# Performance work log

Hardware: AMD Instinct MI355X
Metric: run time of the kernel (lower is better)

## Reference

```python
import jax, jax.numpy as jnp
import numpy as np

N_NODES = 50000
N_EDGES = 1600000
BATCH = 1
CHANNELS = 32


def setup_inputs() -> dict:
    key = jax.random.key(0)
    k1, k2, k3, k4 = jax.random.split(key, 4)
    x = jax.random.normal(k1, (BATCH, CHANNELS, N_NODES), dtype=jnp.float32)
    W = jax.random.uniform(k2, (N_NODES,), dtype=jnp.float32)
    iInd = jax.random.randint(k3, (N_EDGES,), 0, N_NODES)
    jInd = jax.random.randint(k4, (N_EDGES,), 0, N_NODES)
    return {"x": x, "W": W, "iInd": iInd, "jInd": jInd, "nnodes": N_NODES}


def reference(x, W, iInd, jInd, nnodes):
    # neighborNode: gather source-node features along edges, weighted by W[iInd]
    # (branch: W.shape[0] == x.shape[2] == nnodes)
    Wi = W[iInd]                      # [E]
    g = Wi * x[:, :, jInd]            # [B, C, E]
    # neighborEdge: scatter-add W[iInd] * g back to target nodes iInd
    # (branch: W.shape[0] == nnodes != E)
    out = jnp.zeros((x.shape[0], x.shape[1], nnodes), dtype=x.dtype)
    out = out.at[:, :, iInd].add(Wi * g)  # [B, C, nnodes]
    return out
```

## Files before the change

kernel.cpp:

```cpp
#include <hip/hip_runtime.h>
#include <math.h>


#define TCH 32
#define BSHIFT 7
#define BNODES 128
#define MAXNB 512
#define SLOTS 32
#define BIN_THREADS 512
#define TILE 4096
#define SR_THREADS 512
#define SPLIT2 4
#define NSUB 32
#define CMP_CAP 1536
#define SJ_CAP 1536

__device__ __forceinline__ unsigned short f32_to_bf16(float f) {
    unsigned int u = __float_as_uint(f);
    unsigned int r = (u + 0x7FFFu + ((u >> 16) & 1u)) >> 16;
    return (unsigned short)r;
}

__global__ void transpose_CN_to_NC_bf16(const float* __restrict__ x,
                                        unsigned short* __restrict__ xtb,
                                        int* __restrict__ gcursor,
                                        int NB, int N) {
    __shared__ float tile[32][33];
    const int tx = threadIdx.x;
    const int ty = threadIdx.y;
    if (blockIdx.x == 0) {
        const int flat = ty * 32 + tx;
        for (int k = flat; k < NB + 1; k += 1024) gcursor[k] = 0;
    }
    const int n0 = blockIdx.x * 32;
    const int n = n0 + tx;
    if (n < N) tile[ty][tx] = x[(size_t)ty * N + n];
    __syncthreads();
    const int nw = n0 + ty;
    if (nw < N) xtb[(size_t)nw * TCH + tx] = f32_to_bf16(tile[tx][ty]);
}

__device__ __forceinline__ void push_ovf(int* ovf_cnt, int2* ovf, int ovf_cap,
                                         int i, int j) {
    const int p = atomicAdd(ovf_cnt, 1);
    if (p < ovf_cap) ovf[p] = make_int2(i, j);
}

__global__ __launch_bounds__(BIN_THREADS) void bin_edges(
    const int* __restrict__ iInd, const int* __restrict__ jInd,
    int* __restrict__ bins, int* __restrict__ gcursor,
    int* __restrict__ ovf_cnt, int2* __restrict__ ovf, int ovf_cap,
    int E, int NB, int cap) {
    __shared__ int stage[MAXNB * SLOTS];
    __shared__ int scnt[MAXNB];
    __shared__ int sums[BIN_THREADS];
    __shared__ unsigned short excl[MAXNB];
    __shared__ unsigned short gbase[MAXNB];
    __shared__ unsigned short bidx[TILE];
    const int tid = threadIdx.x;

    scnt[tid] = 0;
    __syncthreads();

    const int base = blockIdx.x * TILE + tid * 8;
#pragma unroll
    for (int q = 0; q < 2; ++q) {
        const int eb = base + q * 4;
        if (eb + 3 < E) {
            const int4 iv = *(const int4*)(iInd + eb);
            const int4 jv = *(const int4*)(jInd + eb);
            const int is[4] = {iv.x, iv.y, iv.z, iv.w};
            const int js[4] = {jv.x, jv.y, jv.z, jv.w};
#pragma unroll
            for (int k = 0; k < 4; ++k) {
                const int i = is[k], j = js[k];
                const int b = i >> BSHIFT;
                const int slot = atomicAdd(&scnt[b], 1);
                if (slot < SLOTS)
                    stage[b * SLOTS + slot] = ((i & (BNODES - 1)) << 16) | j;
                else
                    push_ovf(ovf_cnt, ovf, ovf_cap, i, j);
            }
        } else {
            for (int k = 0; k < 4; ++k) {
                const int e = eb + k;
                if (e < E) {
                    const int i = iInd[e], j = jInd[e];
                    const int b = i >> BSHIFT;
                    const int slot = atomicAdd(&scnt[b], 1);
                    if (slot < SLOTS)
                        stage[b * SLOTS + slot] = ((i & (BNODES - 1)) << 16) | j;
                    else
                        push_ovf(ovf_cnt, ovf, ovf_cap, i, j);
                }
            }
        }
    }
    __syncthreads();

    const int cb = min(scnt[tid], SLOTS);
    sums[tid] = cb;
    __syncthreads();
    for (int off = 1; off < BIN_THREADS; off <<= 1) {
        const int v = (tid >= off) ? sums[tid - off] : 0;
        __syncthreads();
        sums[tid] += v;
        __syncthreads();
    }
    const int run0 = sums[tid] - cb;
    const int total = sums[BIN_THREADS - 1];
    excl[tid] = (unsigned short)run0;
    if (cb > 0) {
        gbase[tid] = (unsigned short)atomicAdd(&gcursor[tid], cb);
        for (int t = 0; t < cb; ++t)
            bidx[run0 + t] = (unsigned short)tid;
    }
    __syncthreads();

    for (int idx = tid; idx < total; idx += BIN_THREADS) {
        const int b = bidx[idx];
        const int k = idx - (int)excl[b];
        const int rec = stage[b * SLOTS + k];
        const int gslot = (int)gbase[b] + k;
        if (gslot < cap) {
            bins[(size_t)b * cap + gslot] = rec;
        } else {
            push_ovf(ovf_cnt, ovf, ovf_cap,
                     (b << BSHIFT) | (rec >> 16), rec & 0xFFFF);
        }
    }
}

__global__ __launch_bounds__(SR_THREADS) void sort_reduce5(
    const int* __restrict__ bins, const int* __restrict__ gcursor,
    const unsigned short* __restrict__ xtb, const float* __restrict__ W,
    float* __restrict__ out, int* __restrict__ ovf_cnt,
    int2* __restrict__ ovf, int ovf_cap, int N, int cap) {
    const int bucket = blockIdx.x >> 2;
    const int sub = blockIdx.x & (SPLIT2 - 1);
    __shared__ unsigned int cmp[CMP_CAP];
    __shared__ unsigned short sj[SJ_CAP];
    __shared__ float acc[NSUB * 33];
    __shared__ int hcnt[NSUB];
    __shared__ int off2[NSUB + 1];
    __shared__ int cur[NSUB];
    __shared__ int ccnt;

    int cnt = gcursor[bucket];
    if (cnt > cap) cnt = cap;
    const int* rec = bins + (size_t)bucket * cap;

    if (threadIdx.x < NSUB) { hcnt[threadIdx.x] = 0; cur[threadIdx.x] = 0; }
    if (threadIdx.x == 0) ccnt = 0;
    __syncthreads();

    for (int r = threadIdx.x; r < cnt; r += SR_THREADS) {
        const unsigned int pr = (unsigned int)rec[r];
        const int il = (int)(pr >> 16);
        if ((il >> 5) == sub) {
            const int p = atomicAdd(&ccnt, 1);
            if (p < CMP_CAP) {
                cmp[p] = pr;
                atomicAdd(&hcnt[il & (NSUB - 1)], 1);
            } else {
                push_ovf(ovf_cnt, ovf, ovf_cap,
                         (bucket << BSHIFT) | il, (int)(pr & 0xFFFF));
            }
        }
    }
    __syncthreads();

    if (threadIdx.x == 0) {
        int run = 0;
        for (int k = 0; k < NSUB; ++k) { off2[k] = run; run += hcnt[k]; }
        off2[NSUB] = run;
    }
    __syncthreads();

    const int cc = min(ccnt, CMP_CAP);
    for (int r = threadIdx.x; r < cc; r += SR_THREADS) {
        const unsigned int pr = cmp[r];
        const int il = (int)(pr >> 16) & (NSUB - 1);
        const int pos = off2[il] + atomicAdd(&cur[il], 1);
        sj[pos] = (unsigned short)(pr & 0xFFFF);
    }
    __syncthreads();

    const int lane = threadIdx.x & 31;
    const int g = threadIdx.x >> 5;
    const int rslot = lane >> 3;
    const int c4 = (lane & 7) * 4;
    for (int ill = g; ill < NSUB; ill += SR_THREADS / 32) {
        const int beg = off2[ill];
        const int end = off2[ill + 1];
        float a0 = 0.f, a1 = 0.f, a2 = 0.f, a3 = 0.f;
        int rb = beg;
        for (; rb + 8 <= end; rb += 8) {
            const int j0 = sj[rb + rslot];
            const int j1 = sj[rb + 4 + rslot];
            const uint2 u0 = *(const uint2*)(xtb + (size_t)j0 * TCH + c4);
            const uint2 u1 = *(const uint2*)(xtb + (size_t)j1 * TCH + c4);
            a0 += __uint_as_float(u0.x << 16);
            a1 += __uint_as_float(u0.x & 0xFFFF0000u);
            a2 += __uint_as_float(u0.y << 16);
            a3 += __uint_as_float(u0.y & 0xFFFF0000u);
            a0 += __uint_as_float(u1.x << 16);
            a1 += __uint_as_float(u1.x & 0xFFFF0000u);
            a2 += __uint_as_float(u1.y << 16);
            a3 += __uint_as_float(u1.y & 0xFFFF0000u);
        }
        {
            const int rr = rb + rslot;
            if (rr < end) {
                const int j = sj[rr];
                const uint2 u = *(const uint2*)(xtb + (size_t)j * TCH + c4);
                a0 += __uint_as_float(u.x << 16);
                a1 += __uint_as_float(u.x & 0xFFFF0000u);
                a2 += __uint_as_float(u.y << 16);
                a3 += __uint_as_float(u.y & 0xFFFF0000u);
            }
            const int rr2 = rb + 4 + rslot;
            if (rr2 < end) {
                const int j = sj[rr2];
                const uint2 u = *(const uint2*)(xtb + (size_t)j * TCH + c4);
                a0 += __uint_as_float(u.x << 16);
                a1 += __uint_as_float(u.x & 0xFFFF0000u);
                a2 += __uint_as_float(u.y << 16);
                a3 += __uint_as_float(u.y & 0xFFFF0000u);
            }
        }
        a0 += __shfl_xor(a0, 8);  a1 += __shfl_xor(a1, 8);
        a2 += __shfl_xor(a2, 8);  a3 += __shfl_xor(a3, 8);
        a0 += __shfl_xor(a0, 16); a1 += __shfl_xor(a1, 16);
        a2 += __shfl_xor(a2, 16); a3 += __shfl_xor(a3, 16);
        if (rslot == 0) {
            float* ap = &acc[ill * 33 + c4];
            ap[0] = a0; ap[1] = a1; ap[2] = a2; ap[3] = a3;
        }
    }
    __syncthreads();

    const int i0 = (bucket << BSHIFT) + sub * NSUB;
    for (int k = threadIdx.x; k < NSUB * TCH; k += SR_THREADS) {
        const int ill = k & (NSUB - 1);
        const int cc2 = k >> 5;
        const int i = i0 + ill;
        if (i < N) {
            const float w = W[i];
            out[(size_t)cc2 * N + i] = w * w * acc[ill * 33 + cc2];
        }
    }
}

__global__ void overflow_apply(const int2* __restrict__ ovf,
                               const int* __restrict__ ovf_cnt,
                               const float* __restrict__ W,
                               const float* __restrict__ x,
                               float* __restrict__ out, int N, int ovf_cap) {
    int cnt = *ovf_cnt;
    if (cnt > ovf_cap) cnt = ovf_cap;
    const long long total = (long long)cnt * TCH;
    const long long stride = (long long)gridDim.x * blockDim.x;
    for (long long t = (long long)blockIdx.x * blockDim.x + threadIdx.x;
         t < total; t += stride) {
        const int e = (int)(t >> 5);
        const int c = (int)(t & 31);
        const int2 p = ovf[e];
        const float w = W[p.x];
        atomicAdd(&out[(size_t)c * N + p.x], w * w * x[(size_t)c * N + p.y]);
    }
}

__global__ void edge_scatter_cn(const int* __restrict__ iInd,
                                const int* __restrict__ jInd,
                                const float* __restrict__ W,
                                const float* __restrict__ x,
                                float* __restrict__ out, int E, int N) {
    const long long t = (long long)blockIdx.x * blockDim.x + threadIdx.x;
    const int e = (int)(t >> 5);
    const int c = (int)(t & 31);
    if (e < E) {
        const int i = iInd[e];
        const int j = jInd[e];
        const float w = W[i];
        atomicAdd(&out[(size_t)c * N + i], w * w * x[(size_t)c * N + j]);
    }
}

extern "C" void kernel_launch(void* const* d_in, const int* in_sizes, int n_in,
                              void* d_out, int out_size, void* d_ws, size_t ws_size,
                              hipStream_t stream) {
    const float* x    = (const float*)d_in[0];
    const float* W    = (const float*)d_in[1];
    const int*   iInd = (const int*)d_in[2];
    const int*   jInd = (const int*)d_in[3];

    const int N = in_sizes[1];
    const int E = in_sizes[2];
    float* out = (float*)d_out;

    const int NB = (N + BNODES - 1) >> BSHIFT;
    const int mean = (NB > 0) ? (E / NB) : 0;
    const int cap = mean + (int)(8.0 * sqrt((double)(mean > 0 ? mean : 1))) + 64;

    const size_t A = 256;
    const size_t xtb_bytes = (((size_t)N * TCH * 2) + A - 1) / A * A;
    const size_t bin_bytes = (((size_t)NB * cap * 4) + A - 1) / A * A;
    const size_t cur_bytes = (((size_t)(NB + 1) * 4) + A - 1) / A * A;
    const size_t base_need = xtb_bytes + bin_bytes + cur_bytes;

    int ovf_cap = 0;
    if (ws_size > base_need) {
        size_t avail = ws_size - base_need;
        size_t oc = avail / sizeof(int2);
        if (oc > (size_t)(1 << 21)) oc = (size_t)(1 << 21);
        ovf_cap = (int)oc;
    }

    if (ws_size >= base_need && ovf_cap >= 65536 && NB <= MAXNB &&
        N <= 65536 && cap < 60000) {
        char* wsb = (char*)d_ws;
        unsigned short* xtb = (unsigned short*)wsb;
        int*   bins    = (int*)(wsb + xtb_bytes);
        int*   gcursor = (int*)(wsb + xtb_bytes + bin_bytes);
        int*   ovf_cnt = gcursor + NB;
        int2*  ovf     = (int2*)(wsb + base_need);

        const int ntiles = (N + 31) / 32;
        dim3 tb(32, 32);
        transpose_CN_to_NC_bf16<<<ntiles, tb, 0, stream>>>(
            x, xtb, gcursor, NB, N);

        const int bin_blocks = (E + TILE - 1) / TILE;
        bin_edges<<<bin_blocks, BIN_THREADS, 0, stream>>>(
            iInd, jInd, bins, gcursor, ovf_cnt, ovf, ovf_cap, E, NB, cap);

        sort_reduce5<<<NB * SPLIT2, SR_THREADS, 0, stream>>>(
            bins, gcursor, xtb, W, out, ovf_cnt, ovf, ovf_cap, N, cap);

        overflow_apply<<<128, 256, 0, stream>>>(
            ovf, ovf_cnt, W, x, out, N, ovf_cap);
    } else {
        hipMemsetAsync(out, 0, (size_t)out_size * sizeof(float), stream);
        const int threads = 256;
        const long long total = (long long)E * TCH;
        const int blocks = (int)((total + threads - 1) / threads);
        edge_scatter_cn<<<blocks, threads, 0, stream>>>(iInd, jInd, W, x, out, E, N);
    }
}
```

Baseline: 54.25 us.

## Halve sort-reduce bucket split, vectorize bin record loads, shrink bin staging slots

```diff
diff --git a/kernel.cpp b/kernel.cpp
--- a/kernel.cpp
+++ b/kernel.cpp
@@ -6,14 +6,14 @@
 #define BSHIFT 7
 #define BNODES 128
 #define MAXNB 512
-#define SLOTS 32
+#define SLOTS 16
 #define BIN_THREADS 512
 #define TILE 4096
 #define SR_THREADS 512
-#define SPLIT2 4
-#define NSUB 32
-#define CMP_CAP 1536
-#define SJ_CAP 1536
+#define SPLIT2 2
+#define NSUB 64
+#define CMP_CAP 3072
+#define SJ_CAP 3072
 
 __device__ __forceinline__ unsigned short f32_to_bf16(float f) {
     unsigned int u = __float_as_uint(f);
@@ -131,12 +131,12 @@
     }
 }
 
-__global__ __launch_bounds__(SR_THREADS) void sort_reduce5(
+__global__ __launch_bounds__(SR_THREADS) void sort_reduce6(
     const int* __restrict__ bins, const int* __restrict__ gcursor,
     const unsigned short* __restrict__ xtb, const float* __restrict__ W,
     float* __restrict__ out, int* __restrict__ ovf_cnt,
     int2* __restrict__ ovf, int ovf_cap, int N, int cap) {
-    const int bucket = blockIdx.x >> 2;
+    const int bucket = blockIdx.x >> 1;
     const int sub = blockIdx.x & (SPLIT2 - 1);
     __shared__ unsigned int cmp[CMP_CAP];
     __shared__ unsigned short sj[SJ_CAP];
@@ -154,10 +154,32 @@
     if (threadIdx.x == 0) ccnt = 0;
     __syncthreads();
 
-    for (int r = threadIdx.x; r < cnt; r += SR_THREADS) {
+    const int cnt4 = cnt >> 2;
+    const int4* rec4 = (const int4*)rec;
+    for (int r = threadIdx.x; r < cnt4; r += SR_THREADS) {
+        const int4 v = rec4[r];
+        const unsigned int prs[4] = {(unsigned int)v.x, (unsigned int)v.y,
+                                     (unsigned int)v.z, (unsigned int)v.w};
+#pragma unroll
+        for (int k = 0; k < 4; ++k) {
+            const unsigned int pr = prs[k];
+            const int il = (int)(pr >> 16);
+            if ((il >> 6) == sub) {
+                const int p = atomicAdd(&ccnt, 1);
+                if (p < CMP_CAP) {
+                    cmp[p] = pr;
+                    atomicAdd(&hcnt[il & (NSUB - 1)], 1);
+                } else {
+                    push_ovf(ovf_cnt, ovf, ovf_cap,
+                             (bucket << BSHIFT) | il, (int)(pr & 0xFFFF));
+                }
+            }
+        }
+    }
+    for (int r = (cnt4 << 2) + threadIdx.x; r < cnt; r += SR_THREADS) {
         const unsigned int pr = (unsigned int)rec[r];
         const int il = (int)(pr >> 16);
-        if ((il >> 5) == sub) {
+        if ((il >> 6) == sub) {
             const int p = atomicAdd(&ccnt, 1);
             if (p < CMP_CAP) {
                 cmp[p] = pr;
@@ -243,7 +265,7 @@
     const int i0 = (bucket << BSHIFT) + sub * NSUB;
     for (int k = threadIdx.x; k < NSUB * TCH; k += SR_THREADS) {
         const int ill = k & (NSUB - 1);
-        const int cc2 = k >> 5;
+        const int cc2 = k >> 6;
         const int i = i0 + ill;
         if (i < N) {
             const float w = W[i];
@@ -301,7 +323,8 @@
 
     const int NB = (N + BNODES - 1) >> BSHIFT;
     const int mean = (NB > 0) ? (E / NB) : 0;
-    const int cap = mean + (int)(8.0 * sqrt((double)(mean > 0 ? mean : 1))) + 64;
+    int cap = mean + (int)(8.0 * sqrt((double)(mean > 0 ? mean : 1))) + 64;
+    cap = (cap + 3) & ~3;
 
     const size_t A = 256;
     const size_t xtb_bytes = (((size_t)N * TCH * 2) + A - 1) / A * A;
@@ -335,7 +358,7 @@
         bin_edges<<<bin_blocks, BIN_THREADS, 0, stream>>>(
             iInd, jInd, bins, gcursor, ovf_cnt, ovf, ovf_cap, E, NB, cap);
 
-        sort_reduce5<<<NB * SPLIT2, SR_THREADS, 0, stream>>>(
+        sort_reduce6<<<NB * SPLIT2, SR_THREADS, 0, stream>>>(
             bins, gcursor, xtb, W, out, ovf_cnt, ovf, ovf_cap, N, cap);
 
         overflow_apply<<<128, 256, 0, stream>>>(
```

After: 124.1 us. 129% more time.
